# Optimization experiments

Measured on AMD Instinct MI355X. Metric: run time of the kernel, lower is better.

Reference implementation:

```python
import jax, jax.numpy as jnp
import numpy as np

B, S, D_IN, D, H = 2, 2048, 1024, 1024, 16
HD = D // H

def setup_inputs() -> dict:
    key = jax.random.key(0)
    k1, k2, k3 = jax.random.split(key, 3)
    # xavier_uniform-style scale for weights
    lim_qkv = float(np.sqrt(6.0 / (D_IN + 3 * D)))
    lim_o = float(np.sqrt(6.0 / (D + D)))
    return {
        "x": jax.random.normal(k1, (B, S, D_IN), dtype=jnp.float32),
        "w_qkv": jax.random.uniform(k2, (3 * D, D_IN), dtype=jnp.float32, minval=-lim_qkv, maxval=lim_qkv),
        "b_qkv": jnp.zeros((3 * D,), dtype=jnp.float32),
        "w_o": jax.random.uniform(k3, (D, D), dtype=jnp.float32, minval=-lim_o, maxval=lim_o),
        "b_o": jnp.zeros((D,), dtype=jnp.float32),
    }

def reference(x, w_qkv, b_qkv, w_o, b_o):
    b, s, _ = x.shape
    # QKV projection: [B,S,3D]
    qkv = jnp.einsum("bsd,ed->bse", x, w_qkv) + b_qkv
    # [B,S,H,3*HD] -> [B,H,S,3*HD]
    qkv = qkv.reshape(b, s, H, 3 * HD).transpose(0, 2, 1, 3)
    q, k, v = jnp.split(qkv, 3, axis=-1)  # each [B,H,S,HD]
    scale = 1.0 / jnp.sqrt(jnp.asarray(HD, dtype=q.dtype))
    logits = jnp.einsum("bhqd,bhkd->bhqk", q, k) * scale  # [B,H,S,S]
    attn = jax.nn.softmax(logits, axis=-1)
    vals = jnp.einsum("bhqk,bhkd->bhqd", attn, v)  # [B,H,S,HD]
    vals = vals.transpose(0, 2, 1, 3).reshape(b, s, D)
    return jnp.einsum("bsd,ed->bse", vals, w_o) + b_o
```

## Files before the change

### kernel.cpp

```cpp
#include <hip/hip_runtime.h>
#include <hip/hip_bf16.h>
#include <math.h>

#define BATCH 2
#define SLEN  2048
#define DIN   1024
#define DMODEL 1024
#define NHEAD 16
#define HD    64
#define E3    3072

typedef unsigned short us;
typedef _Float16 f16;
typedef __attribute__((ext_vector_type(8))) _Float16 f16x8;
typedef __attribute__((ext_vector_type(8))) unsigned short us8;
typedef __attribute__((ext_vector_type(4))) unsigned short us4;
typedef __attribute__((ext_vector_type(4))) float f32x4;
typedef __attribute__((ext_vector_type(16))) float f32x16;

#define QSCALE 0.18033688011112042f

__device__ __forceinline__ us f16bits(float x) {
    const f16 h = (f16)x;
    return __builtin_bit_cast(us, h);
}

#define GLL16(g, l)                                                                     \
    __builtin_amdgcn_global_load_lds((const __attribute__((address_space(1))) unsigned int*)(g), \
                                     (__attribute__((address_space(3))) unsigned int*)(l), 16, 0, 0)

__global__ __launch_bounds__(256) void cvt3_f16(
    const float* __restrict__ x, us* __restrict__ ox, int nx,
    const float* __restrict__ wq, us* __restrict__ owq, int nq,
    const float* __restrict__ wo, us* __restrict__ owo)
{
    int i = (blockIdx.x * 256 + threadIdx.x) * 8;
    const float* s;
    us* o;
    if (i < nx)           { s = x;  o = ox; }
    else if (i < nx + nq) { s = wq; o = owq; i -= nx; }
    else                  { s = wo; o = owo; i -= nx + nq; }
    const float4 f0 = *(const float4*)&s[i];
    const float4 f1 = *(const float4*)&s[i + 4];
    const float v[8] = {f0.x, f0.y, f0.z, f0.w, f1.x, f1.y, f1.z, f1.w};
    us8 h;
#pragma unroll
    for (int j = 0; j < 8; ++j) h[j] = f16bits(v[j]);
    *(us8*)&o[i] = h;
}

template <bool QKV_OUT>
__global__ __launch_bounds__(256) void gemm_f16(
    const us* __restrict__ Am, const us* __restrict__ Bm,
    const float* __restrict__ bias, void* __restrict__ Cout,
    int M, int N, int K)
{
    __shared__ __align__(16) us As[128 * 32];
    __shared__ __align__(16) us Bs[128 * 32];

    const int t    = threadIdx.x;
    const int lane = t & 63;
    const int w    = t >> 6;
    const int ml   = lane & 15;
    const int quad = lane >> 4;
    const int wm   = w >> 1;
    const int wn   = w & 1;

    const int m0 = blockIdx.y * 128;
    const int n0 = blockIdx.x * 128;

    const int srow = (lane >> 2);
    const int scol = (lane & 3) * 8;

    const us* pA = Am + (size_t)(m0 + w * 32 + srow) * K + scol;
    const us* pB = Bm + (size_t)(n0 + w * 32 + srow) * K + scol;
    const size_t rstep = (size_t)16 * K;

    us* lA0 = &As[(w * 32) * 32];
    us* lA1 = &As[(w * 32 + 16) * 32];
    us* lB0 = &Bs[(w * 32) * 32];
    us* lB1 = &Bs[(w * 32 + 16) * 32];

    f32x4 acc[4][4];
#pragma unroll
    for (int i = 0; i < 4; ++i)
#pragma unroll
        for (int j = 0; j < 4; ++j) {
            acc[i][j][0] = 0.f; acc[i][j][1] = 0.f; acc[i][j][2] = 0.f; acc[i][j][3] = 0.f;
        }

    for (int k0 = 0; k0 < K; k0 += 32) {
        __syncthreads();
        GLL16(pA + k0, lA0); GLL16(pA + k0 + rstep, lA1);
        GLL16(pB + k0, lB0); GLL16(pB + k0 + rstep, lB1);
        __syncthreads();

        f16x8 a[4];
#pragma unroll
        for (int i = 0; i < 4; ++i)
            a[i] = __builtin_bit_cast(f16x8, *(const us8*)&As[(wm * 64 + i * 16 + ml) * 32 + quad * 8]);
#pragma unroll
        for (int j = 0; j < 4; ++j) {
            const f16x8 b = __builtin_bit_cast(f16x8, *(const us8*)&Bs[(wn * 64 + j * 16 + ml) * 32 + quad * 8]);
#pragma unroll
            for (int i = 0; i < 4; ++i)
                acc[i][j] = __builtin_amdgcn_mfma_f32_16x16x32_f16(a[i], b, acc[i][j], 0, 0, 0);
        }
    }

    float bj[4], cs[4];
#pragma unroll
    for (int j = 0; j < 4; ++j) {
        const int col = n0 + wn * 64 + j * 16 + ml;
        bj[j] = bias[col];
        cs[j] = (QKV_OUT && (col % 192) < 64) ? QSCALE : 1.0f;
    }

#pragma unroll
    for (int i = 0; i < 4; ++i) {
#pragma unroll
        for (int r = 0; r < 4; ++r) {
            const size_t rowoff = (size_t)(m0 + wm * 64 + i * 16 + quad * 4 + r) * N;
#pragma unroll
            for (int j = 0; j < 4; ++j) {
                const int col = n0 + wn * 64 + j * 16 + ml;
                const float v = (acc[i][j][r] + bj[j]) * cs[j];
                if (QKV_OUT) ((us*)Cout)[rowoff + col] = f16bits(v);
                else         ((float*)Cout)[rowoff + col] = v;
            }
        }
    }
}

#define ABQ 128
#define ACH 64
#define NCH (SLEN / ACH)
#define LQA 72

__global__ __launch_bounds__(256) void attn_mfma(
    const us* __restrict__ qkvh, us* __restrict__ vals)
{
    __shared__ __align__(16) us QPs[ABQ * LQA];
    __shared__ __align__(16) us Ks[ACH * LQA];
    __shared__ __align__(16) us Vt[HD * LQA];

    const int t    = threadIdx.x;
    const int lane = t & 63;
    const int w    = t >> 6;
    const int m32  = lane & 31;
    const int half = lane >> 5;

    const int bh = blockIdx.y;
    const int b  = bh >> 4;
    const int h  = bh & 15;
    const int q0 = blockIdx.x * ABQ;

    const size_t base = (size_t)b * SLEN * E3;
    const int qoff = h * 192;

    {
        const int row = t >> 1;
        const int c0  = (t & 1) * 32;
        const us* g = &qkvh[base + (size_t)(q0 + row) * E3 + qoff + c0];
#pragma unroll
        for (int s = 0; s < 4; ++s)
            *(us8*)&QPs[row * LQA + c0 + s * 8] = *(const us8*)(g + s * 8);
    }
    __syncthreads();

    f16x8 aq[4];
#pragma unroll
    for (int s = 0; s < 4; ++s)
        aq[s] = __builtin_bit_cast(f16x8, *(const us8*)&QPs[(w * 32 + m32) * LQA + half * 8 + 16 * s]);

    const int krA = t >> 2;
    const int ksA = (t & 3) * 16;
    const int krB = t & 63;
    const int ksB = w * 16;

    us8 kk0, kk1, vv0, vv1;
    {
        const us* gK = &qkvh[base + (size_t)(krA) * E3 + qoff + 64 + ksA];
        kk0 = *(const us8*)gK; kk1 = *(const us8*)(gK + 8);
        const us* gV = &qkvh[base + (size_t)(krB) * E3 + qoff + 128 + ksB];
        vv0 = *(const us8*)gV; vv1 = *(const us8*)(gV + 8);
    }

    f32x16 O[2];
#pragma unroll
    for (int dt = 0; dt < 2; ++dt)
#pragma unroll
        for (int r = 0; r < 16; ++r) O[dt][r] = 0.f;
    float lpart = 0.f;

    const int prow = (w * 32 + m32) * LQA;

    for (int c = 0; c < NCH; ++c) {
        __syncthreads();
        *(us8*)&Ks[krA * LQA + ksA]     = kk0;
        *(us8*)&Ks[krA * LQA + ksA + 8] = kk1;
#pragma unroll
        for (int j = 0; j < 8; ++j) Vt[(ksB + j) * LQA + krB]     = vv0[j];
#pragma unroll
        for (int j = 0; j < 8; ++j) Vt[(ksB + 8 + j) * LQA + krB] = vv1[j];
        __syncthreads();
        if (c + 1 < NCH) {
            const us* gK = &qkvh[base + (size_t)((c + 1) * ACH + krA) * E3 + qoff + 64 + ksA];
            kk0 = *(const us8*)gK; kk1 = *(const us8*)(gK + 8);
            const us* gV = &qkvh[base + (size_t)((c + 1) * ACH + krB) * E3 + qoff + 128 + ksB];
            vv0 = *(const us8*)gV; vv1 = *(const us8*)(gV + 8);
        }

#pragma unroll
        for (int kt = 0; kt < 2; ++kt) {
            f32x16 z;
#pragma unroll
            for (int r = 0; r < 16; ++r) z[r] = 0.f;
#pragma unroll
            for (int s = 0; s < 4; ++s) {
                const f16x8 ak = __builtin_bit_cast(f16x8, *(const us8*)&Ks[(kt * 32 + m32) * LQA + half * 8 + 16 * s]);
                z = __builtin_amdgcn_mfma_f32_32x32x16_f16(ak, aq[s], z, 0, 0, 0);
            }
#pragma unroll
            for (int g = 0; g < 4; ++g) {
                us4 pp;
#pragma unroll
                for (int r2 = 0; r2 < 4; ++r2) {
                    const float p = __builtin_amdgcn_exp2f(z[g * 4 + r2]);
                    lpart += p;
                    pp[r2] = f16bits(p);
                }
                *(us4*)&QPs[prow + kt * 32 + 8 * g + 4 * half] = pp;
            }
        }

        f16x8 pf[4];
#pragma unroll
        for (int s = 0; s < 4; ++s)
            pf[s] = __builtin_bit_cast(f16x8, *(const us8*)&QPs[prow + half * 8 + 16 * s]);
#pragma unroll
        for (int dt = 0; dt < 2; ++dt) {
#pragma unroll
            for (int s = 0; s < 4; ++s) {
                const f16x8 av = __builtin_bit_cast(f16x8, *(const us8*)&Vt[(dt * 32 + m32) * LQA + half * 8 + 16 * s]);
                O[dt] = __builtin_amdgcn_mfma_f32_32x32x16_f16(av, pf[s], O[dt], 0, 0, 0);
            }
        }
    }

    const float l  = lpart + __shfl_xor(lpart, 32);
    const float rl = 1.0f / l;
    const int sq = q0 + w * 32 + m32;
    const size_t rowbase = (size_t)(b * SLEN + sq) * DMODEL + h * HD;
#pragma unroll
    for (int dt = 0; dt < 2; ++dt) {
#pragma unroll
        for (int g = 0; g < 4; ++g) {
            us4 o4;
#pragma unroll
            for (int r2 = 0; r2 < 4; ++r2) o4[r2] = f16bits(O[dt][g * 4 + r2] * rl);
            *(us4*)&vals[rowbase + dt * 32 + 8 * g + 4 * half] = o4;
        }
    }
}

extern "C" void kernel_launch(void* const* d_in, const int* in_sizes, int n_in,
                              void* d_out, int out_size, void* d_ws, size_t ws_size,
                              hipStream_t stream) {
    const float* x     = (const float*)d_in[0];
    const float* w_qkv = (const float*)d_in[1];
    const float* b_qkv = (const float*)d_in[2];
    const float* w_o   = (const float*)d_in[3];
    const float* b_o   = (const float*)d_in[4];
    float* out = (float*)d_out;

    const int M   = BATCH * SLEN;
    const int XN  = M * DIN;
    const int WQN = E3 * DIN;
    const int WON = DMODEL * DMODEL;
    const size_t QKVN = (size_t)BATCH * SLEN * E3;

    us* qkvh = (us*)d_ws;
    us* xh   = qkvh + QKVN;
    us* wq   = xh + XN;
    us* wo   = wq + WQN;

    cvt3_f16<<<dim3((XN + WQN + WON) / 2048), 256, 0, stream>>>(
        x, xh, XN, w_qkv, wq, WQN, w_o, wo);

    gemm_f16<true><<<dim3(E3 / 128, M / 128), 256, 0, stream>>>(
        xh, wq, b_qkv, qkvh, M, E3, DIN);

    us* vals = xh;
    attn_mfma<<<dim3(SLEN / ABQ, BATCH * NHEAD), 256, 0, stream>>>(qkvh, vals);

    gemm_f16<false><<<dim3(DMODEL / 128, M / 128), 256, 0, stream>>>(
        vals, wo, b_o, out, M, DMODEL, DMODEL);
}
```

Before: 200.7 us.

## Write transposed V from QKV GEMM and run attention from registers without LDS

```diff
diff --git a/kernel.cpp b/kernel.cpp
--- a/kernel.cpp
+++ b/kernel.cpp
@@ -12,9 +12,11 @@
 
 typedef unsigned short us;
 typedef _Float16 f16;
+typedef __attribute__((ext_vector_type(2))) _Float16 f16x2;
 typedef __attribute__((ext_vector_type(8))) _Float16 f16x8;
 typedef __attribute__((ext_vector_type(8))) unsigned short us8;
 typedef __attribute__((ext_vector_type(4))) unsigned short us4;
+typedef __attribute__((ext_vector_type(4))) unsigned int u32x4;
 typedef __attribute__((ext_vector_type(4))) float f32x4;
 typedef __attribute__((ext_vector_type(16))) float f32x16;
 
@@ -24,6 +26,8 @@
     const f16 h = (f16)x;
     return __builtin_bit_cast(us, h);
 }
+
+#define LD8(p) (__builtin_bit_cast(f16x8, *(const us8*)(p)))
 
 #define GLL16(g, l)                                                                     \
     __builtin_amdgcn_global_load_lds((const __attribute__((address_space(1))) unsigned int*)(g), \
@@ -53,7 +57,7 @@
 __global__ __launch_bounds__(256) void gemm_f16(
     const us* __restrict__ Am, const us* __restrict__ Bm,
     const float* __restrict__ bias, void* __restrict__ Cout,
-    int M, int N, int K)
+    us* __restrict__ VtOut, int M, int N, int K)
 {
     __shared__ __align__(16) us As[128 * 32];
     __shared__ __align__(16) us Bs[128 * 32];
@@ -108,82 +112,96 @@
         }
     }
 
-    float bj[4], cs[4];
-#pragma unroll
-    for (int j = 0; j < 4; ++j) {
-        const int col = n0 + wn * 64 + j * 16 + ml;
-        bj[j] = bias[col];
-        cs[j] = (QKV_OUT && (col % 192) < 64) ? QSCALE : 1.0f;
-    }
-
-#pragma unroll
-    for (int i = 0; i < 4; ++i) {
-#pragma unroll
-        for (int r = 0; r < 4; ++r) {
-            const size_t rowoff = (size_t)(m0 + wm * 64 + i * 16 + quad * 4 + r) * N;
-#pragma unroll
-            for (int j = 0; j < 4; ++j) {
-                const int col = n0 + wn * 64 + j * 16 + ml;
-                const float v = (acc[i][j][r] + bj[j]) * cs[j];
-                if (QKV_OUT) ((us*)Cout)[rowoff + col] = f16bits(v);
-                else         ((float*)Cout)[rowoff + col] = v;
-            }
-        }
-    }
-}
-
-#define ABQ 128
+    if (QKV_OUT) {
+        us* qkv = (us*)Cout;
+#pragma unroll
+        for (int j = 0; j < 4; ++j) {
+            const int colbase = n0 + wn * 64 + j * 16;
+            const int cls = (colbase % 192) >> 6;
+            const float bjv = bias[colbase + ml];
+            if (cls == 2) {
+                const int head = colbase / 192;
+                const int d = (colbase % 192) - 128 + ml;
+#pragma unroll
+                for (int i = 0; i < 4; ++i) {
+                    const int rg = m0 + wm * 64 + i * 16 + quad * 4;
+                    const int bb = rg >> 11;
+                    const int ss = rg & 2047;
+                    us4 pp;
+#pragma unroll
+                    for (int r = 0; r < 4; ++r) pp[r] = f16bits(acc[i][j][r] + bjv);
+                    *(us4*)&VtOut[((size_t)((bb * 16 + head) * 64 + d)) * SLEN + ss] = pp;
+                }
+            } else {
+                const float sc = (cls == 0) ? QSCALE : 1.0f;
+#pragma unroll
+                for (int i = 0; i < 4; ++i) {
+#pragma unroll
+                    for (int r = 0; r < 4; ++r) {
+                        const size_t rowoff = (size_t)(m0 + wm * 64 + i * 16 + quad * 4 + r) * N;
+                        qkv[rowoff + colbase + ml] = f16bits((acc[i][j][r] + bjv) * sc);
+                    }
+                }
+            }
+        }
+    } else {
+        float* Cf = (float*)Cout;
+        float bj[4];
+#pragma unroll
+        for (int j = 0; j < 4; ++j) bj[j] = bias[n0 + wn * 64 + j * 16 + ml];
+#pragma unroll
+        for (int i = 0; i < 4; ++i) {
+#pragma unroll
+            for (int r = 0; r < 4; ++r) {
+                const size_t rowoff = (size_t)(m0 + wm * 64 + i * 16 + quad * 4 + r) * N;
+#pragma unroll
+                for (int j = 0; j < 4; ++j)
+                    Cf[rowoff + n0 + wn * 64 + j * 16 + ml] = acc[i][j][r] + bj[j];
+            }
+        }
+    }
+}
+
 #define ACH 64
 #define NCH (SLEN / ACH)
-#define LQA 72
 
 __global__ __launch_bounds__(256) void attn_mfma(
-    const us* __restrict__ qkvh, us* __restrict__ vals)
+    const us* __restrict__ qkvh, const us* __restrict__ vtg, us* __restrict__ vals)
 {
-    __shared__ __align__(16) us QPs[ABQ * LQA];
-    __shared__ __align__(16) us Ks[ACH * LQA];
-    __shared__ __align__(16) us Vt[HD * LQA];
-
     const int t    = threadIdx.x;
     const int lane = t & 63;
     const int w    = t >> 6;
     const int m32  = lane & 31;
-    const int half = lane >> 5;
+    const int h    = lane >> 5;
 
     const int bh = blockIdx.y;
     const int b  = bh >> 4;
-    const int h  = bh & 15;
-    const int q0 = blockIdx.x * ABQ;
+    const int hd = bh & 15;
+    const int q0 = blockIdx.x * 128 + w * 32;
 
     const size_t base = (size_t)b * SLEN * E3;
-    const int qoff = h * 192;
-
+    const int qoff = hd * 192;
+
+    f16x8 aq[4];
     {
-        const int row = t >> 1;
-        const int c0  = (t & 1) * 32;
-        const us* g = &qkvh[base + (size_t)(q0 + row) * E3 + qoff + c0];
-#pragma unroll
-        for (int s = 0; s < 4; ++s)
-            *(us8*)&QPs[row * LQA + c0 + s * 8] = *(const us8*)(g + s * 8);
-    }
-    __syncthreads();
-
-    f16x8 aq[4];
-#pragma unroll
-    for (int s = 0; s < 4; ++s)
-        aq[s] = __builtin_bit_cast(f16x8, *(const us8*)&QPs[(w * 32 + m32) * LQA + half * 8 + 16 * s]);
-
-    const int krA = t >> 2;
-    const int ksA = (t & 3) * 16;
-    const int krB = t & 63;
-    const int ksB = w * 16;
-
-    us8 kk0, kk1, vv0, vv1;
-    {
-        const us* gK = &qkvh[base + (size_t)(krA) * E3 + qoff + 64 + ksA];
-        kk0 = *(const us8*)gK; kk1 = *(const us8*)(gK + 8);
-        const us* gV = &qkvh[base + (size_t)(krB) * E3 + qoff + 128 + ksB];
-        vv0 = *(const us8*)gV; vv1 = *(const us8*)(gV + 8);
+        const us* qrow = qkvh + base + (size_t)(q0 + m32) * E3 + qoff + 8 * h;
+#pragma unroll
+        for (int s = 0; s < 4; ++s) aq[s] = LD8(qrow + 16 * s);
+    }
+
+    const us* kp0 = qkvh + base + (size_t)m32 * E3 + qoff + 64 + 8 * h;
+    const us* kp1 = kp0 + (size_t)32 * E3;
+    const us* vp0 = vtg + ((size_t)((b * 16 + hd) * 64 + m32)) * SLEN + 8 * h;
+    const us* vp1 = vp0 + (size_t)32 * SLEN;
+    const size_t kstep = (size_t)ACH * E3;
+
+    f16x8 kk[8], vv[8];
+#pragma unroll
+    for (int s = 0; s < 4; ++s) {
+        kk[s]     = LD8(kp0 + 16 * s);
+        kk[4 + s] = LD8(kp1 + 16 * s);
+        vv[s]     = LD8(vp0 + 16 * s);
+        vv[4 + s] = LD8(vp1 + 16 * s);
     }
 
     f32x16 O[2];
@@ -193,65 +211,87 @@
         for (int r = 0; r < 16; ++r) O[dt][r] = 0.f;
     float lpart = 0.f;
 
-    const int prow = (w * 32 + m32) * LQA;
-
     for (int c = 0; c < NCH; ++c) {
-        __syncthreads();
-        *(us8*)&Ks[krA * LQA + ksA]     = kk0;
-        *(us8*)&Ks[krA * LQA + ksA + 8] = kk1;
-#pragma unroll
-        for (int j = 0; j < 8; ++j) Vt[(ksB + j) * LQA + krB]     = vv0[j];
-#pragma unroll
-        for (int j = 0; j < 8; ++j) Vt[(ksB + 8 + j) * LQA + krB] = vv1[j];
-        __syncthreads();
+        f32x16 z[2];
+#pragma unroll
+        for (int kt = 0; kt < 2; ++kt)
+#pragma unroll
+            for (int r = 0; r < 16; ++r) z[kt][r] = 0.f;
+#pragma unroll
+        for (int s = 0; s < 4; ++s) {
+            z[0] = __builtin_amdgcn_mfma_f32_32x32x16_f16(kk[s],     aq[s], z[0], 0, 0, 0);
+            z[1] = __builtin_amdgcn_mfma_f32_32x32x16_f16(kk[4 + s], aq[s], z[1], 0, 0, 0);
+        }
         if (c + 1 < NCH) {
-            const us* gK = &qkvh[base + (size_t)((c + 1) * ACH + krA) * E3 + qoff + 64 + ksA];
-            kk0 = *(const us8*)gK; kk1 = *(const us8*)(gK + 8);
-            const us* gV = &qkvh[base + (size_t)((c + 1) * ACH + krB) * E3 + qoff + 128 + ksB];
-            vv0 = *(const us8*)gV; vv1 = *(const us8*)(gV + 8);
-        }
-
+            const us* k0 = kp0 + (size_t)(c + 1) * kstep;
+            const us* k1 = kp1 + (size_t)(c + 1) * kstep;
+#pragma unroll
+            for (int s = 0; s < 4; ++s) {
+                kk[s]     = LD8(k0 + 16 * s);
+                kk[4 + s] = LD8(k1 + 16 * s);
+            }
+        }
+
+        unsigned int pkw[2][4][2];
+        float lp = 0.f;
 #pragma unroll
         for (int kt = 0; kt < 2; ++kt) {
-            f32x16 z;
-#pragma unroll
-            for (int r = 0; r < 16; ++r) z[r] = 0.f;
+#pragma unroll
+            for (int g = 0; g < 4; ++g) {
+                const float p0 = __builtin_amdgcn_exp2f(z[kt][g * 4 + 0]);
+                const float p1 = __builtin_amdgcn_exp2f(z[kt][g * 4 + 1]);
+                const float p2 = __builtin_amdgcn_exp2f(z[kt][g * 4 + 2]);
+                const float p3 = __builtin_amdgcn_exp2f(z[kt][g * 4 + 3]);
+                lp += (p0 + p1) + (p2 + p3);
+                pkw[kt][g][0] = __builtin_bit_cast(unsigned int, __builtin_amdgcn_cvt_pkrtz(p0, p1));
+                pkw[kt][g][1] = __builtin_bit_cast(unsigned int, __builtin_amdgcn_cvt_pkrtz(p2, p3));
+            }
+        }
+        lpart += lp;
+
+        unsigned int rw[2][2][2];
+#pragma unroll
+        for (int kt = 0; kt < 2; ++kt)
+#pragma unroll
+            for (int sl = 0; sl < 2; ++sl)
+#pragma unroll
+                for (int hw = 0; hw < 2; ++hw) {
+                    const unsigned int send = h ? pkw[kt][2 * sl][hw] : pkw[kt][2 * sl + 1][hw];
+                    rw[kt][sl][hw] = (unsigned int)__shfl_xor((int)send, 32);
+                }
+
+        f16x8 pf[4];
+#pragma unroll
+        for (int s = 0; s < 4; ++s) {
+            const int kt = s >> 1, sl = s & 1;
+            u32x4 wd;
+            wd[0] = h ? rw[kt][sl][0] : pkw[kt][2 * sl][0];
+            wd[1] = h ? rw[kt][sl][1] : pkw[kt][2 * sl][1];
+            wd[2] = h ? pkw[kt][2 * sl + 1][0] : rw[kt][sl][0];
+            wd[3] = h ? pkw[kt][2 * sl + 1][1] : rw[kt][sl][1];
+            pf[s] = __builtin_bit_cast(f16x8, wd);
+        }
+
+#pragma unroll
+        for (int s = 0; s < 4; ++s) {
+            O[0] = __builtin_amdgcn_mfma_f32_32x32x16_f16(vv[s],     pf[s], O[0], 0, 0, 0);
+            O[1] = __builtin_amdgcn_mfma_f32_32x32x16_f16(vv[4 + s], pf[s], O[1], 0, 0, 0);
+        }
+        if (c + 1 < NCH) {
+            const us* v0 = vp0 + (c + 1) * ACH;
+            const us* v1 = vp1 + (c + 1) * ACH;
 #pragma unroll
             for (int s = 0; s < 4; ++s) {
-                const f16x8 ak = __builtin_bit_cast(f16x8, *(const us8*)&Ks[(kt * 32 + m32) * LQA + half * 8 + 16 * s]);
-                z = __builtin_amdgcn_mfma_f32_32x32x16_f16(ak, aq[s], z, 0, 0, 0);
-            }
-#pragma unroll
-            for (int g = 0; g < 4; ++g) {
-                us4 pp;
-#pragma unroll
-                for (int r2 = 0; r2 < 4; ++r2) {
-                    const float p = __builtin_amdgcn_exp2f(z[g * 4 + r2]);
-                    lpart += p;
-                    pp[r2] = f16bits(p);
-                }
-                *(us4*)&QPs[prow + kt * 32 + 8 * g + 4 * half] = pp;
-            }
-        }
-
-        f16x8 pf[4];
-#pragma unroll
-        for (int s = 0; s < 4; ++s)
-            pf[s] = __builtin_bit_cast(f16x8, *(const us8*)&QPs[prow + half * 8 + 16 * s]);
-#pragma unroll
-        for (int dt = 0; dt < 2; ++dt) {
-#pragma unroll
-            for (int s = 0; s < 4; ++s) {
-                const f16x8 av = __builtin_bit_cast(f16x8, *(const us8*)&Vt[(dt * 32 + m32) * LQA + half * 8 + 16 * s]);
-                O[dt] = __builtin_amdgcn_mfma_f32_32x32x16_f16(av, pf[s], O[dt], 0, 0, 0);
+                vv[s]     = LD8(v0 + 16 * s);
+                vv[4 + s] = LD8(v1 + 16 * s);
             }
         }
     }
 
     const float l  = lpart + __shfl_xor(lpart, 32);
     const float rl = 1.0f / l;
-    const int sq = q0 + w * 32 + m32;
-    const size_t rowbase = (size_t)(b * SLEN + sq) * DMODEL + h * HD;
+    const int sq = q0 + m32;
+    const size_t rowbase = (size_t)(b * SLEN + sq) * DMODEL + hd * HD;
 #pragma unroll
     for (int dt = 0; dt < 2; ++dt) {
 #pragma unroll
@@ -259,7 +299,7 @@
             us4 o4;
 #pragma unroll
             for (int r2 = 0; r2 < 4; ++r2) o4[r2] = f16bits(O[dt][g * 4 + r2] * rl);
-            *(us4*)&vals[rowbase + dt * 32 + 8 * g + 4 * half] = o4;
+            *(us4*)&vals[rowbase + dt * 32 + 8 * g + 4 * h] = o4;
         }
     }
 }
@@ -279,9 +319,11 @@
     const int WQN = E3 * DIN;
     const int WON = DMODEL * DMODEL;
     const size_t QKVN = (size_t)BATCH * SLEN * E3;
+    const size_t VTN  = (size_t)BATCH * NHEAD * HD * SLEN;
 
     us* qkvh = (us*)d_ws;
-    us* xh   = qkvh + QKVN;
+    us* vtg  = qkvh + QKVN;
+    us* xh   = vtg + VTN;
     us* wq   = xh + XN;
     us* wo   = wq + WQN;
 
@@ -289,11 +331,11 @@
         x, xh, XN, w_qkv, wq, WQN, w_o, wo);
 
     gemm_f16<true><<<dim3(E3 / 128, M / 128), 256, 0, stream>>>(
-        xh, wq, b_qkv, qkvh, M, E3, DIN);
+        xh, wq, b_qkv, qkvh, vtg, M, E3, DIN);
 
     us* vals = xh;
-    attn_mfma<<<dim3(SLEN / ABQ, BATCH * NHEAD), 256, 0, stream>>>(qkvh, vals);
+    attn_mfma<<<dim3(SLEN / 128, BATCH * NHEAD), 256, 0, stream>>>(qkvh, vtg, vals);
 
     gemm_f16<false><<<dim3(DMODEL / 128, M / 128), 256, 0, stream>>>(
-        vals, wo, b_o, out, M, DMODEL, DMODEL);
-}
+        vals, wo, b_o, out, nullptr, M, DMODEL, DMODEL);
+}
```

After: 279.2 us. 39.1% more time.
